# Performance work log

Measured on AMD Instinct MI355X. Metric: run time of the kernel, lower is better.

The kernel has to match this reference:

```python
import jax, jax.numpy as jnp
import numpy as np
import math

T, NE, DA = 4096, 2048, 2048
LAYER_ID, NUM_LAYERS = 12, 24


def setup_inputs() -> dict:
    key = jax.random.key(0)
    kx, kk, kv, kr, ko = jax.random.split(key, 5)
    # --- learned params, initialised exactly like the haiku module ---
    ratio_0_to_1 = LAYER_ID / (NUM_LAYERS - 1)
    ratio_1_to_almost0 = 1.0 - LAYER_ID / NUM_LAYERS
    time_first = jnp.ones(DA, jnp.float32) * math.log(0.3) + \
        jnp.array([(i + 1) % 3 - 1 for i in range(DA)], jnp.float32) * 0.5
    time_decay = -5 + 8 * (jnp.arange(DA, dtype=jnp.float32) / (DA - 1)) ** (0.7 + 1.3 * ratio_0_to_1)
    ddd = jnp.arange(DA, dtype=jnp.float32)[jnp.newaxis, :] / DA  # [1, DA]
    time_mix_k = jnp.power(ddd, ratio_1_to_almost0)
    time_mix_v = time_mix_k + 0.3 * ratio_0_to_1
    time_mix_r = jnp.power(ddd, ratio_1_to_almost0 * 0.5)
    s = 1.0 / math.sqrt(NE)
    return {
        'x': jax.random.normal(kx, (T, NE), jnp.float32),
        'time_first': time_first,
        'time_decay': time_decay,
        'time_mix_k': time_mix_k,
        'time_mix_v': time_mix_v,
        'time_mix_r': time_mix_r,
        'W_key': jax.random.normal(kk, (NE, DA), jnp.float32) * s,
        'W_value': jax.random.normal(kv, (NE, DA), jnp.float32) * s,
        'W_receptance': jax.random.normal(kr, (NE, DA), jnp.float32) * s,
        'W_output': jax.random.normal(ko, (DA, NE), jnp.float32) * (1.0 / math.sqrt(DA)),
    }


def _wkv(time_decay, time_first, k, v):
    # k, v: [T, C]. Vectorized over channels; sequential scan over time.
    dtype = k.dtype
    w = -jnp.exp(time_decay.astype(jnp.float32))  # [C]
    u = time_first.astype(jnp.float32)            # [C]
    kf = k.astype(jnp.float32)
    vf = v.astype(jnp.float32)
    C = kf.shape[1]

    def body(carry, kv):
        p, q, o = carry
        kt, vt = kv
        # output at t (includes bonus u on current token)
        no = jnp.maximum(o, u + kt)
        A = jnp.exp(o - no)
        B = jnp.exp(u + kt - no)
        y = (A * p + B * vt) / (A * q + B)
        # state update (decay w applied to running sums)
        no2 = jnp.maximum(w + o, kt)
        A2 = jnp.exp(w + o - no2)
        B2 = jnp.exp(kt - no2)
        return (A2 * p + B2 * vt, A2 * q + B2, no2), y

    init = (jnp.zeros(C, jnp.float32), jnp.zeros(C, jnp.float32),
            jnp.full(C, -1e38, jnp.float32))
    _, ys = jax.lax.scan(body, init, (kf, vf))  # ys: [T, C]
    return ys.astype(dtype)


def reference(x, time_first, time_decay, time_mix_k, time_mix_v, time_mix_r,
              W_key, W_value, W_receptance, W_output):
    # time shift: shift sequence right by one (zero-pad first position)
    xx = jnp.pad(x, [(1, 0), (0, 0)])[:-1, :]
    xk = x * time_mix_k + xx * (1 - time_mix_k)
    xv = x * time_mix_v + xx * (1 - time_mix_v)
    xr = x * time_mix_r + xx * (1 - time_mix_r)
    k = xk @ W_key          # [T, DA]
    v = xv @ W_value        # [T, DA]
    r = xr @ W_receptance   # [T, DA]
    sr = jax.nn.sigmoid(r)
    wkv = _wkv(time_decay, time_first, k, v)  # [T, DA]
    return (sr * wkv) @ W_output              # [T, NE]
```

## Files before the change

kernel.cpp:

```cpp
#include <hip/hip_runtime.h>
#include <math.h>

#define T_ 4096
#define NE_ 2048
#define DA_ 2048
#define TDA ((size_t)T_ * NE_)

constexpr int NC = 128;
constexpr int CL = T_ / NC;

typedef __attribute__((ext_vector_type(8))) short short8;
typedef __attribute__((ext_vector_type(4))) float f32x4;

__device__ __forceinline__ unsigned short f2bf(float f) {
  union { float f; unsigned int u; } v; v.f = f;
  unsigned int u = v.u;
  return (unsigned short)((u + 0x7FFFu + ((u >> 16) & 1u)) >> 16);
}
__device__ __forceinline__ float bf2f(unsigned short h) {
  union { unsigned int u; float f; } v; v.u = ((unsigned int)h) << 16;
  return v.f;
}

__device__ __forceinline__ void gload_lds16(const void* g, void* l) {
  __builtin_amdgcn_global_load_lds(
      (const __attribute__((address_space(1))) void*)g,
      (__attribute__((address_space(3))) void*)l, 16, 0, 0);
}

__device__ __forceinline__ void gemm_core(
    const unsigned short* __restrict__ A, const unsigned short* __restrict__ Bt,
    void* __restrict__ C, int c_bf16)
{
  constexpr int K = 2048, N = 2048;
  __shared__ unsigned short As[128 * 64];
  __shared__ unsigned short Bs[128 * 64];

  const int tid = threadIdx.x;
  const int w = tid >> 6, lane = tid & 63;
  const int bm = blockIdx.x * 128, bn = blockIdx.y * 128;
  const int wr = w >> 1, wc = w & 1;

  f32x4 acc[4][4];
#pragma unroll
  for (int m = 0; m < 4; ++m)
#pragma unroll
    for (int n = 0; n < 4; ++n) acc[m][n] = (f32x4){0.f, 0.f, 0.f, 0.f};

  const int sr8 = lane >> 3;
  const int gcs = (lane & 7) ^ sr8;
  const size_t gA0 = (size_t)(bm + w * 32 + sr8) * K + gcs * 8;
  const size_t gB0 = (size_t)(bn + w * 32 + sr8) * K + gcs * 8;
  unsigned short* lA = &As[(w * 32) * 64];
  unsigned short* lB = &Bs[(w * 32) * 64];

  const int lr = lane & 15, ck = lane >> 4;
  const int x7 = lr & 7;
  const int arow = wr * 64 + lr;
  const int brow = wc * 64 + lr;

  for (int kk = 0; kk < K; kk += 64) {
    __syncthreads();
#pragma unroll
    for (int g = 0; g < 4; ++g) {
      gload_lds16(A + gA0 + kk + (size_t)(g * 8) * K, lA + g * 512);
      gload_lds16(Bt + gB0 + kk + (size_t)(g * 8) * K, lB + g * 512);
    }
    __syncthreads();

#pragma unroll
    for (int s = 0; s < 2; ++s) {
      const int c0 = ((s * 4 + ck) ^ x7) * 8;
      short8 af[4], bfr[4];
#pragma unroll
      for (int m = 0; m < 4; ++m)
        af[m] = *reinterpret_cast<const short8*>(&As[(arow + m * 16) * 64 + c0]);
#pragma unroll
      for (int n = 0; n < 4; ++n)
        bfr[n] = *reinterpret_cast<const short8*>(&Bs[(brow + n * 16) * 64 + c0]);
#pragma unroll
      for (int m = 0; m < 4; ++m)
#pragma unroll
        for (int n = 0; n < 4; ++n)
          acc[m][n] = __builtin_amdgcn_mfma_f32_16x16x32_bf16(af[m], bfr[n], acc[m][n], 0, 0, 0);
    }
  }

  const int crow0 = bm + wr * 64 + (lane >> 4) * 4;
  const int ccol0 = bn + wc * 64 + (lane & 15);
  if (c_bf16) {
    unsigned short* Cb = (unsigned short*)C;
#pragma unroll
    for (int m = 0; m < 4; ++m)
#pragma unroll
      for (int n = 0; n < 4; ++n)
#pragma unroll
        for (int j = 0; j < 4; ++j)
          Cb[(size_t)(crow0 + m * 16 + j) * N + ccol0 + n * 16] = f2bf(acc[m][n][j]);
  } else {
    float* Cf = (float*)C;
#pragma unroll
    for (int m = 0; m < 4; ++m)
#pragma unroll
      for (int n = 0; n < 4; ++n)
#pragma unroll
        for (int j = 0; j < 4; ++j)
          Cf[(size_t)(crow0 + m * 16 + j) * N + ccol0 + n * 16] = acc[m][n][j];
  }
}

__global__ __launch_bounds__(256) void gemm3_bf16(
    const unsigned short* __restrict__ A0, const unsigned short* __restrict__ A1,
    const unsigned short* __restrict__ A2,
    const unsigned short* __restrict__ B0, const unsigned short* __restrict__ B1,
    const unsigned short* __restrict__ B2,
    void* __restrict__ C0, void* __restrict__ C1, void* __restrict__ C2,
    int c_bf16)
{
  const int z = blockIdx.z;
  const unsigned short* A = (z == 0) ? A0 : (z == 1) ? A1 : A2;
  const unsigned short* B = (z == 0) ? B0 : (z == 1) ? B1 : B2;
  void* C = (z == 0) ? C0 : (z == 1) ? C1 : C2;
  gemm_core(A, B, C, c_bf16);
}

__global__ __launch_bounds__(256) void transpose_cvt3(
    const float* __restrict__ W0, const float* __restrict__ W1,
    const float* __restrict__ W2,
    unsigned short* __restrict__ O0, unsigned short* __restrict__ O1,
    unsigned short* __restrict__ O2)
{
  constexpr int K = 2048, N = 2048;
  const int z = blockIdx.z;
  const float* W = (z == 0) ? W0 : (z == 1) ? W1 : W2;
  unsigned short* O = (z == 0) ? O0 : (z == 1) ? O1 : O2;

  __shared__ float tile[32][33];
  const int bk = blockIdx.y * 32;
  const int bn = blockIdx.x * 32;
  const int tx = threadIdx.x;
  const int ty = threadIdx.y;
#pragma unroll
  for (int i = 0; i < 32; i += 8)
    tile[ty + i][tx] = W[(size_t)(bk + ty + i) * N + bn + tx];
  __syncthreads();
#pragma unroll
  for (int i = 0; i < 32; i += 8)
    O[(size_t)(bn + ty + i) * K + bk + tx] = f2bf(tile[tx][ty + i]);
}

__global__ __launch_bounds__(256) void mix3_cvt(
    const float* __restrict__ x,
    const float* __restrict__ tmk, const float* __restrict__ tmv,
    const float* __restrict__ tmr,
    unsigned short* __restrict__ ok, unsigned short* __restrict__ ov,
    unsigned short* __restrict__ orr)
{
  const int i = blockIdx.x * 256 + threadIdx.x;
  const int t = i / (NE_ / 4);
  const int e4 = i % (NE_ / 4);
  const float4 xc = reinterpret_cast<const float4*>(x)[i];
  float4 xp = make_float4(0.f, 0.f, 0.f, 0.f);
  if (t > 0) xp = reinterpret_cast<const float4*>(x)[i - NE_ / 4];
  const float4 dx = make_float4(xc.x - xp.x, xc.y - xp.y, xc.z - xp.z, xc.w - xp.w);

  float4 m;
  ushort4 r;
  m = reinterpret_cast<const float4*>(tmk)[e4];
  r.x = f2bf(xp.x + m.x * dx.x); r.y = f2bf(xp.y + m.y * dx.y);
  r.z = f2bf(xp.z + m.z * dx.z); r.w = f2bf(xp.w + m.w * dx.w);
  reinterpret_cast<ushort4*>(ok)[i] = r;
  m = reinterpret_cast<const float4*>(tmv)[e4];
  r.x = f2bf(xp.x + m.x * dx.x); r.y = f2bf(xp.y + m.y * dx.y);
  r.z = f2bf(xp.z + m.z * dx.z); r.w = f2bf(xp.w + m.w * dx.w);
  reinterpret_cast<ushort4*>(ov)[i] = r;
  m = reinterpret_cast<const float4*>(tmr)[e4];
  r.x = f2bf(xp.x + m.x * dx.x); r.y = f2bf(xp.y + m.y * dx.y);
  r.z = f2bf(xp.z + m.z * dx.z); r.w = f2bf(xp.w + m.w * dx.w);
  reinterpret_cast<ushort4*>(orr)[i] = r;
}

__global__ __launch_bounds__(64) void wkv_pass1(
    const unsigned short* __restrict__ Kb, const unsigned short* __restrict__ Vb,
    const float* __restrict__ td, float* __restrict__ SP, float* __restrict__ SQ)
{
  const int c4 = blockIdx.x * 64 + threadIdx.x;
  const int chunk = blockIdx.y;
  const int t0 = chunk * CL;
  const float4 tdv = reinterpret_cast<const float4*>(td)[c4];
  float lam[4] = {__expf(-__expf(tdv.x)), __expf(-__expf(tdv.y)),
                  __expf(-__expf(tdv.z)), __expf(-__expf(tdv.w))};
  float P[4] = {0.f, 0.f, 0.f, 0.f}, Q[4] = {0.f, 0.f, 0.f, 0.f};
#pragma unroll 4
  for (int t = t0; t < t0 + CL; ++t) {
    const ushort4 kq = reinterpret_cast<const ushort4*>(Kb + (size_t)t * DA_)[c4];
    const ushort4 vq = reinterpret_cast<const ushort4*>(Vb + (size_t)t * DA_)[c4];
    const float kf[4] = {bf2f(kq.x), bf2f(kq.y), bf2f(kq.z), bf2f(kq.w)};
    const float vf[4] = {bf2f(vq.x), bf2f(vq.y), bf2f(vq.z), bf2f(vq.w)};
#pragma unroll
    for (int j = 0; j < 4; ++j) {
      const float e = __expf(kf[j]);
      P[j] = fmaf(lam[j], P[j], e * vf[j]);
      Q[j] = fmaf(lam[j], Q[j], e);
    }
  }
  reinterpret_cast<float4*>(SP + (size_t)chunk * DA_)[c4] = (float4){P[0], P[1], P[2], P[3]};
  reinterpret_cast<float4*>(SQ + (size_t)chunk * DA_)[c4] = (float4){Q[0], Q[1], Q[2], Q[3]};
}

__global__ __launch_bounds__(256) void wkv_pass2(
    const float* __restrict__ td, float* __restrict__ SP, float* __restrict__ SQ)
{
  const int c = blockIdx.x * 256 + threadIdx.x;
  const float lamL = __expf(-__expf(td[c]) * (float)CL);
  float P = 0.f, Q = 0.f;
  for (int i0 = 0; i0 < NC; i0 += 16) {
    float sp[16], sq[16];
#pragma unroll
    for (int j = 0; j < 16; ++j) {
      sp[j] = SP[(size_t)(i0 + j) * DA_ + c];
      sq[j] = SQ[(size_t)(i0 + j) * DA_ + c];
    }
#pragma unroll
    for (int j = 0; j < 16; ++j) {
      SP[(size_t)(i0 + j) * DA_ + c] = P;
      SQ[(size_t)(i0 + j) * DA_ + c] = Q;
      P = fmaf(lamL, P, sp[j]);
      Q = fmaf(lamL, Q, sq[j]);
    }
  }
}

__global__ __launch_bounds__(64) void wkv_pass3(
    const unsigned short* __restrict__ Kb, const unsigned short* __restrict__ Vb,
    const unsigned short* __restrict__ Rb, unsigned short* __restrict__ Ab,
    const float* __restrict__ td, const float* __restrict__ tf,
    const float* __restrict__ SP, const float* __restrict__ SQ)
{
  const int c4 = blockIdx.x * 64 + threadIdx.x;
  const int chunk = blockIdx.y;
  const int t0 = chunk * CL;
  const float4 tdv = reinterpret_cast<const float4*>(td)[c4];
  const float4 tfv = reinterpret_cast<const float4*>(tf)[c4];
  const float lam[4] = {__expf(-__expf(tdv.x)), __expf(-__expf(tdv.y)),
                        __expf(-__expf(tdv.z)), __expf(-__expf(tdv.w))};
  const float eu[4] = {__expf(tfv.x), __expf(tfv.y), __expf(tfv.z), __expf(tfv.w)};
  const float4 p0 = reinterpret_cast<const float4*>(SP + (size_t)chunk * DA_)[c4];
  const float4 q0 = reinterpret_cast<const float4*>(SQ + (size_t)chunk * DA_)[c4];
  float P[4] = {p0.x, p0.y, p0.z, p0.w};
  float Q[4] = {q0.x, q0.y, q0.z, q0.w};
#pragma unroll 4
  for (int t = t0; t < t0 + CL; ++t) {
    const ushort4 kq = reinterpret_cast<const ushort4*>(Kb + (size_t)t * DA_)[c4];
    const ushort4 vq = reinterpret_cast<const ushort4*>(Vb + (size_t)t * DA_)[c4];
    const ushort4 rq = reinterpret_cast<const ushort4*>(Rb + (size_t)t * DA_)[c4];
    const float kf[4] = {bf2f(kq.x), bf2f(kq.y), bf2f(kq.z), bf2f(kq.w)};
    const float vf[4] = {bf2f(vq.x), bf2f(vq.y), bf2f(vq.z), bf2f(vq.w)};
    const float rf[4] = {bf2f(rq.x), bf2f(rq.y), bf2f(rq.z), bf2f(rq.w)};
    ushort4 a;
    unsigned short* ap = (unsigned short*)&a;
#pragma unroll
    for (int j = 0; j < 4; ++j) {
      const float e = __expf(kf[j]);
      const float b = eu[j] * e;
      const float y = (P[j] + b * vf[j]) / (Q[j] + b);
      const float sr = 1.f / (1.f + __expf(-rf[j]));
      ap[j] = f2bf(sr * y);
      P[j] = fmaf(lam[j], P[j], e * vf[j]);
      Q[j] = fmaf(lam[j], Q[j], e);
    }
    reinterpret_cast<ushort4*>(Ab + (size_t)t * DA_)[c4] = a;
  }
}

extern "C" void kernel_launch(void* const* d_in, const int* in_sizes, int n_in,
                              void* d_out, int out_size, void* d_ws, size_t ws_size,
                              hipStream_t stream)
{
  const float* x   = (const float*)d_in[0];
  const float* tf  = (const float*)d_in[1];
  const float* td  = (const float*)d_in[2];
  const float* tmk = (const float*)d_in[3];
  const float* tmv = (const float*)d_in[4];
  const float* tmr = (const float*)d_in[5];
  const float* Wk  = (const float*)d_in[6];
  const float* Wv  = (const float*)d_in[7];
  const float* Wr  = (const float*)d_in[8];
  const float* Wo  = (const float*)d_in[9];
  float* out = (float*)d_out;

  const size_t MB = 1024 * 1024;
  char* ws = (char*)d_ws;

  const dim3 blk(256);
  const dim3 wblk(64);
  const dim3 tblk(32, 8);
  const dim3 ggrid1(T_ / 128, DA_ / 128, 1);
  const dim3 wgrid(DA_ / 4 / 64, NC);
  const size_t NEED_BATCH = 122 * MB;

  if (ws_size >= NEED_BATCH) {
    unsigned short* xmk = (unsigned short*)(ws + 0 * MB);
    unsigned short* xmv = (unsigned short*)(ws + 16 * MB);
    unsigned short* xmr = (unsigned short*)(ws + 32 * MB);
    unsigned short* WtK = (unsigned short*)(ws + 48 * MB);
    unsigned short* WtV = (unsigned short*)(ws + 56 * MB);
    unsigned short* WtR = (unsigned short*)(ws + 64 * MB);
    unsigned short* kb  = (unsigned short*)(ws + 72 * MB);
    unsigned short* vb  = (unsigned short*)(ws + 88 * MB);
    unsigned short* rb  = (unsigned short*)(ws + 104 * MB);
    float* sp = (float*)(ws + 120 * MB);
    float* sq = (float*)(ws + 121 * MB);

    transpose_cvt3<<<dim3(64, 64, 3), tblk, 0, stream>>>(Wk, Wv, Wr, WtK, WtV, WtR);
    mix3_cvt<<<TDA / 4 / 256, blk, 0, stream>>>(x, tmk, tmv, tmr, xmk, xmv, xmr);
    gemm3_bf16<<<dim3(T_ / 128, DA_ / 128, 3), blk, 0, stream>>>(
        xmk, xmv, xmr, WtK, WtV, WtR, kb, vb, rb, 1);

    transpose_cvt3<<<dim3(64, 64, 1), tblk, 0, stream>>>(Wo, Wo, Wo, WtK, WtK, WtK);

    wkv_pass1<<<wgrid, wblk, 0, stream>>>(kb, vb, td, sp, sq);
    wkv_pass2<<<dim3(DA_ / 256), blk, 0, stream>>>(td, sp, sq);
    wkv_pass3<<<wgrid, wblk, 0, stream>>>(kb, vb, rb, xmk, td, tf, sp, sq);

    gemm3_bf16<<<ggrid1, blk, 0, stream>>>(xmk, xmk, xmk, WtK, WtK, WtK, out, out, out, 0);
  } else {
    unsigned short* xmk = (unsigned short*)(ws + 0 * MB);
    unsigned short* xmv = (unsigned short*)(ws + 16 * MB);
    unsigned short* xmr = (unsigned short*)(ws + 32 * MB);
    unsigned short* Wt  = (unsigned short*)(ws + 48 * MB);
    unsigned short* kb  = (unsigned short*)(ws + 56 * MB);
    unsigned short* vb  = (unsigned short*)(ws + 72 * MB);
    unsigned short* rb  = (unsigned short*)(ws + 88 * MB);
    float* sp = (float*)(ws + 104 * MB);
    float* sq = (float*)(ws + 105 * MB);

    mix3_cvt<<<TDA / 4 / 256, blk, 0, stream>>>(x, tmk, tmv, tmr, xmk, xmv, xmr);
    transpose_cvt3<<<dim3(64, 64, 1), tblk, 0, stream>>>(Wk, Wk, Wk, Wt, Wt, Wt);
    gemm3_bf16<<<ggrid1, blk, 0, stream>>>(xmk, xmk, xmk, Wt, Wt, Wt, kb, kb, kb, 1);
    transpose_cvt3<<<dim3(64, 64, 1), tblk, 0, stream>>>(Wv, Wv, Wv, Wt, Wt, Wt);
    gemm3_bf16<<<ggrid1, blk, 0, stream>>>(xmv, xmv, xmv, Wt, Wt, Wt, vb, vb, vb, 1);
    transpose_cvt3<<<dim3(64, 64, 1), tblk, 0, stream>>>(Wr, Wr, Wr, Wt, Wt, Wt);
    gemm3_bf16<<<ggrid1, blk, 0, stream>>>(xmr, xmr, xmr, Wt, Wt, Wt, rb, rb, rb, 1);

    wkv_pass1<<<wgrid, wblk, 0, stream>>>(kb, vb, td, sp, sq);
    wkv_pass2<<<dim3(DA_ / 256), blk, 0, stream>>>(td, sp, sq);
    wkv_pass3<<<wgrid, wblk, 0, stream>>>(kb, vb, rb, xmk, td, tf, sp, sq);

    transpose_cvt3<<<dim3(64, 64, 1), tblk, 0, stream>>>(Wo, Wo, Wo, Wt, Wt, Wt);
    gemm3_bf16<<<ggrid1, blk, 0, stream>>>(xmk, xmk, xmk, Wt, Wt, Wt, out, out, out, 0);
  }
}
```

Before: 350.0 us.

## Vectorize weight transpose-convert and double WKV scan chunk count with larger blocks

Rewrites the weight transpose/bf16 conversion to use 64x64 tiles with float4 loads, converting to bf16 before staging in shared memory and writing ushort4 stores. Doubles the number of WKV scan chunks and uses 256-thread blocks with deeper unrolling to raise the number of active waves on the sequential-per-chunk scan. Relocates the chunk-state buffers into the space of a weight buffer that is no longer needed, shrinking the workspace requirement. More chunks add work to the carry-propagation pass and more state traffic.

Measured after the change: 356.0 us. No clear change (+1.7%).

```diff
diff --git a/kernel.cpp b/kernel.cpp
--- a/kernel.cpp
+++ b/kernel.cpp
@@ -6,7 +6,7 @@
 #define DA_ 2048
 #define TDA ((size_t)T_ * NE_)
 
-constexpr int NC = 128;
+constexpr int NC = 256;
 constexpr int CL = T_ / NC;
 
 typedef __attribute__((ext_vector_type(8))) short short8;
@@ -130,23 +130,39 @@
     unsigned short* __restrict__ O0, unsigned short* __restrict__ O1,
     unsigned short* __restrict__ O2)
 {
-  constexpr int K = 2048, N = 2048;
   const int z = blockIdx.z;
   const float* W = (z == 0) ? W0 : (z == 1) ? W1 : W2;
   unsigned short* O = (z == 0) ? O0 : (z == 1) ? O1 : O2;
 
-  __shared__ float tile[32][33];
-  const int bk = blockIdx.y * 32;
-  const int bn = blockIdx.x * 32;
-  const int tx = threadIdx.x;
-  const int ty = threadIdx.y;
-#pragma unroll
-  for (int i = 0; i < 32; i += 8)
-    tile[ty + i][tx] = W[(size_t)(bk + ty + i) * N + bn + tx];
+  __shared__ unsigned short tileT[64][68];
+  const int bk = blockIdx.y * 64;
+  const int bn = blockIdx.x * 64;
+  const int u = threadIdx.x;
+
+  {
+    const int r = u >> 2;
+    const int c0 = (u & 3) * 16;
+    const float4* src = reinterpret_cast<const float4*>(
+        &W[(size_t)(bk + r) * 2048 + bn + c0]);
+#pragma unroll
+    for (int j = 0; j < 4; ++j) {
+      const float4 f = src[j];
+      tileT[c0 + j * 4 + 0][r] = f2bf(f.x);
+      tileT[c0 + j * 4 + 1][r] = f2bf(f.y);
+      tileT[c0 + j * 4 + 2][r] = f2bf(f.z);
+      tileT[c0 + j * 4 + 3][r] = f2bf(f.w);
+    }
+  }
   __syncthreads();
 #pragma unroll
-  for (int i = 0; i < 32; i += 8)
-    O[(size_t)(bn + ty + i) * K + bk + tx] = f2bf(tile[tx][ty + i]);
+  for (int p = 0; p < 4; ++p) {
+    const int n = p * 16 + (u >> 4);
+    const int k0 = (u & 15) * 4;
+    ushort4 o;
+    o.x = tileT[n][k0 + 0]; o.y = tileT[n][k0 + 1];
+    o.z = tileT[n][k0 + 2]; o.w = tileT[n][k0 + 3];
+    *reinterpret_cast<ushort4*>(&O[(size_t)(bn + n) * 2048 + bk + k0]) = o;
+  }
 }
 
 __global__ __launch_bounds__(256) void mix3_cvt(
@@ -180,18 +196,18 @@
   reinterpret_cast<ushort4*>(orr)[i] = r;
 }
 
-__global__ __launch_bounds__(64) void wkv_pass1(
+__global__ __launch_bounds__(256) void wkv_pass1(
     const unsigned short* __restrict__ Kb, const unsigned short* __restrict__ Vb,
     const float* __restrict__ td, float* __restrict__ SP, float* __restrict__ SQ)
 {
-  const int c4 = blockIdx.x * 64 + threadIdx.x;
+  const int c4 = blockIdx.x * 256 + threadIdx.x;
   const int chunk = blockIdx.y;
   const int t0 = chunk * CL;
   const float4 tdv = reinterpret_cast<const float4*>(td)[c4];
   float lam[4] = {__expf(-__expf(tdv.x)), __expf(-__expf(tdv.y)),
                   __expf(-__expf(tdv.z)), __expf(-__expf(tdv.w))};
   float P[4] = {0.f, 0.f, 0.f, 0.f}, Q[4] = {0.f, 0.f, 0.f, 0.f};
-#pragma unroll 4
+#pragma unroll 8
   for (int t = t0; t < t0 + CL; ++t) {
     const ushort4 kq = reinterpret_cast<const ushort4*>(Kb + (size_t)t * DA_)[c4];
     const ushort4 vq = reinterpret_cast<const ushort4*>(Vb + (size_t)t * DA_)[c4];
@@ -231,13 +247,13 @@
   }
 }
 
-__global__ __launch_bounds__(64) void wkv_pass3(
+__global__ __launch_bounds__(256) void wkv_pass3(
     const unsigned short* __restrict__ Kb, const unsigned short* __restrict__ Vb,
     const unsigned short* __restrict__ Rb, unsigned short* __restrict__ Ab,
     const float* __restrict__ td, const float* __restrict__ tf,
     const float* __restrict__ SP, const float* __restrict__ SQ)
 {
-  const int c4 = blockIdx.x * 64 + threadIdx.x;
+  const int c4 = blockIdx.x * 256 + threadIdx.x;
   const int chunk = blockIdx.y;
   const int t0 = chunk * CL;
   const float4 tdv = reinterpret_cast<const float4*>(td)[c4];
@@ -293,11 +309,10 @@
   char* ws = (char*)d_ws;
 
   const dim3 blk(256);
-  const dim3 wblk(64);
-  const dim3 tblk(32, 8);
+  const dim3 tgrid3(32, 32, 3), tgrid1(32, 32, 1);
   const dim3 ggrid1(T_ / 128, DA_ / 128, 1);
-  const dim3 wgrid(DA_ / 4 / 64, NC);
-  const size_t NEED_BATCH = 122 * MB;
+  const dim3 wgrid(DA_ / 4 / 256, NC);
+  const size_t NEED_BATCH = 120 * MB;
 
   if (ws_size >= NEED_BATCH) {
     unsigned short* xmk = (unsigned short*)(ws + 0 * MB);
@@ -309,19 +324,19 @@
     unsigned short* kb  = (unsigned short*)(ws + 72 * MB);
     unsigned short* vb  = (unsigned short*)(ws + 88 * MB);
     unsigned short* rb  = (unsigned short*)(ws + 104 * MB);
-    float* sp = (float*)(ws + 120 * MB);
-    float* sq = (float*)(ws + 121 * MB);
-
-    transpose_cvt3<<<dim3(64, 64, 3), tblk, 0, stream>>>(Wk, Wv, Wr, WtK, WtV, WtR);
+    float* sp = (float*)(ws + 56 * MB);
+    float* sq = (float*)(ws + 58 * MB);
+
+    transpose_cvt3<<<tgrid3, blk, 0, stream>>>(Wk, Wv, Wr, WtK, WtV, WtR);
     mix3_cvt<<<TDA / 4 / 256, blk, 0, stream>>>(x, tmk, tmv, tmr, xmk, xmv, xmr);
     gemm3_bf16<<<dim3(T_ / 128, DA_ / 128, 3), blk, 0, stream>>>(
         xmk, xmv, xmr, WtK, WtV, WtR, kb, vb, rb, 1);
 
-    transpose_cvt3<<<dim3(64, 64, 1), tblk, 0, stream>>>(Wo, Wo, Wo, WtK, WtK, WtK);
-
-    wkv_pass1<<<wgrid, wblk, 0, stream>>>(kb, vb, td, sp, sq);
+    transpose_cvt3<<<tgrid1, blk, 0, stream>>>(Wo, Wo, Wo, WtK, WtK, WtK);
+
+    wkv_pass1<<<wgrid, blk, 0, stream>>>(kb, vb, td, sp, sq);
     wkv_pass2<<<dim3(DA_ / 256), blk, 0, stream>>>(td, sp, sq);
-    wkv_pass3<<<wgrid, wblk, 0, stream>>>(kb, vb, rb, xmk, td, tf, sp, sq);
+    wkv_pass3<<<wgrid, blk, 0, stream>>>(kb, vb, rb, xmk, td, tf, sp, sq);
 
     gemm3_bf16<<<ggrid1, blk, 0, stream>>>(xmk, xmk, xmk, WtK, WtK, WtK, out, out, out, 0);
   } else {
@@ -333,21 +348,21 @@
     unsigned short* vb  = (unsigned short*)(ws + 72 * MB);
     unsigned short* rb  = (unsigned short*)(ws + 88 * MB);
     float* sp = (float*)(ws + 104 * MB);
-    float* sq = (float*)(ws + 105 * MB);
+    float* sq = (float*)(ws + 106 * MB);
 
     mix3_cvt<<<TDA / 4 / 256, blk, 0, stream>>>(x, tmk, tmv, tmr, xmk, xmv, xmr);
-    transpose_cvt3<<<dim3(64, 64, 1), tblk, 0, stream>>>(Wk, Wk, Wk, Wt, Wt, Wt);
+    transpose_cvt3<<<tgrid1, blk, 0, stream>>>(Wk, Wk, Wk, Wt, Wt, Wt);
     gemm3_bf16<<<ggrid1, blk, 0, stream>>>(xmk, xmk, xmk, Wt, Wt, Wt, kb, kb, kb, 1);
-    transpose_cvt3<<<dim3(64, 64, 1), tblk, 0, stream>>>(Wv, Wv, Wv, Wt, Wt, Wt);
+    transpose_cvt3<<<tgrid1, blk, 0, stream>>>(Wv, Wv, Wv, Wt, Wt, Wt);
     gemm3_bf16<<<ggrid1, blk, 0, stream>>>(xmv, xmv, xmv, Wt, Wt, Wt, vb, vb, vb, 1);
-    transpose_cvt3<<<dim3(64, 64, 1), tblk, 0, stream>>>(Wr, Wr, Wr, Wt, Wt, Wt);
+    transpose_cvt3<<<tgrid1, blk, 0, stream>>>(Wr, Wr, Wr, Wt, Wt, Wt);
     gemm3_bf16<<<ggrid1, blk, 0, stream>>>(xmr, xmr, xmr, Wt, Wt, Wt, rb, rb, rb, 1);
 
-    wkv_pass1<<<wgrid, wblk, 0, stream>>>(kb, vb, td, sp, sq);
+    wkv_pass1<<<wgrid, blk, 0, stream>>>(kb, vb, td, sp, sq);
     wkv_pass2<<<dim3(DA_ / 256), blk, 0, stream>>>(td, sp, sq);
-    wkv_pass3<<<wgrid, wblk, 0, stream>>>(kb, vb, rb, xmk, td, tf, sp, sq);
-
-    transpose_cvt3<<<dim3(64, 64, 1), tblk, 0, stream>>>(Wo, Wo, Wo, Wt, Wt, Wt);
+    wkv_pass3<<<wgrid, blk, 0, stream>>>(kb, vb, rb, xmk, td, tf, sp, sq);
+
+    transpose_cvt3<<<tgrid1, blk, 0, stream>>>(Wo, Wo, Wo, Wt, Wt, Wt);
     gemm3_bf16<<<ggrid1, blk, 0, stream>>>(xmk, xmk, xmk, Wt, Wt, Wt, out, out, out, 0);
   }
 }
```
